# Optimization experiments

Measured on AMD Instinct MI355X. Metric: run time of the kernel, lower is better.

The kernel has to match this reference:

```python
import jax, jax.numpy as jnp
import numpy as np

# sigmas (defaults from the module)
VAR_0, VAR_A, VAR_B = 1.0, 1.0, 0.0

def V_phi(a, b, c):
    # default id_phi: (a, b, c) -> b, where Sigma = [[a, b], [b, c]]
    return b


def setup_inputs() -> dict:
    key = jax.random.key(0)
    kx, ky = jax.random.split(key)
    B, T, D = 128, 1024, 64
    dt = 1.0 / (T - 1)
    scale = np.sqrt(dt / D).astype(np.float32)
    # Brownian-like paths: increments ~ N(0, dt/D) so quadratic variation is O(1)
    # and the multiplicative kernel recurrence stays numerically bounded.
    X = jnp.cumsum(jax.random.normal(kx, (B, T, D), jnp.float32) * scale, axis=1)
    Y = jnp.cumsum(jax.random.normal(ky, (B, T, D), jnp.float32) * scale, axis=1)
    return {"X": X, "Y": Y}


def _kernel_same(dd):
    # dd: (b, T-1) = <dX_t, dX_t> / dt ; returns Kxx: (b, T)
    def step(k, d_t):
        k_new = k + (VAR_A * V_phi(k, k, k) + VAR_B) * d_t
        return k_new, k_new
    k0 = jnp.full((dd.shape[0],), VAR_0, dd.dtype)
    _, ks = jax.lax.scan(step, k0, dd.T)           # ks: (T-1, b)
    return jnp.concatenate([k0[None, :], ks], axis=0).T  # (b, T)


def reference(X, Y):
    bx, T, d = X.shape
    by = Y.shape[0]
    interval = jnp.linspace(0.0, 1.0, T).astype(X.dtype)
    dt = jnp.diff(interval)                         # (T-1,)
    dX = jnp.diff(X, axis=1)                        # (bx, T-1, d)
    dY = jnp.diff(Y, axis=1)                        # (by, T-1, d)

    dXdX = (dX * dX).sum(-1) / dt                   # (bx, T-1)
    dYdY = (dY * dY).sum(-1) / dt                   # (by, T-1)
    dXdY = jnp.einsum('itd,jtd->ijt', dX, dY) / dt  # (bx, by, T-1)

    Kxx = _kernel_same(dXdX)                        # (bx, T)
    Kyy = _kernel_same(dYdY)                        # (by, T)

    def step(k, inp):
        kxx_t, kyy_t, dxy_t = inp                   # (bx,), (by,), (bx, by)
        k_new = k + (VAR_A * V_phi(kxx_t[:, None], k, kyy_t[None, :]) + VAR_B) * dxy_t
        return k_new, k_new

    k0 = jnp.full((bx, by), VAR_0, X.dtype)
    xs = (Kxx[:, :-1].T, Kyy[:, :-1].T, jnp.moveaxis(dXdY, 2, 0))
    _, ks = jax.lax.scan(step, k0, xs)              # (T-1, bx, by)
    K = jnp.concatenate([k0[None], ks], axis=0)     # (T, bx, by)
    return jnp.moveaxis(K, 0, 2)                    # (bx, by, T)
```

## Files before the change

kernel.cpp:

```cpp
#include <hip/hip_runtime.h>

typedef __attribute__((ext_vector_type(8))) short short8;
typedef __attribute__((ext_vector_type(4))) float floatx4;

constexpr int BX    = 128;
constexpr int TT    = 1024;
constexpr int DDIM  = 64;
constexpr int NPAIR = BX * BX;
constexpr int LCH   = 16;
constexpr int NCH   = TT / LCH;
constexpr float DT_INV = 1023.0f;

__device__ __forceinline__ int sidxE(int row, int k) {
    return row * 64 + ((((k >> 3) ^ (row & 7)) << 3) | (k & 7));
}

__device__ __forceinline__ ushort f2bf(float f) {
    uint u = __builtin_bit_cast(uint, f);
    u += 0x7fffu + ((u >> 16) & 1u);
    return (ushort)(u >> 16);
}

__device__ __forceinline__ void cvt_store(ushort* hiP, ushort* loP, const float* v) {
    uint hw[4], lw[4];
#pragma unroll
    for (int p = 0; p < 4; ++p) {
        const ushort h0 = f2bf(v[2 * p]), h1 = f2bf(v[2 * p + 1]);
        const float r0 = v[2 * p]     - __builtin_bit_cast(float, (uint)h0 << 16);
        const float r1 = v[2 * p + 1] - __builtin_bit_cast(float, (uint)h1 << 16);
        const ushort l0 = f2bf(r0), l1 = f2bf(r1);
        hw[p] = (uint)h0 | ((uint)h1 << 16);
        lw[p] = (uint)l0 | ((uint)l1 << 16);
    }
    *(uint4*)hiP = make_uint4(hw[0], hw[1], hw[2], hw[3]);
    *(uint4*)loP = make_uint4(lw[0], lw[1], lw[2], lw[3]);
}

__device__ __forceinline__ void ld8(const float* p, float* dst) {
    const float4 a = *(const float4*)p;
    const float4 b = *(const float4*)(p + 4);
    dst[0] = a.x; dst[1] = a.y; dst[2] = a.z; dst[3] = a.w;
    dst[4] = b.x; dst[5] = b.y; dst[6] = b.z; dst[7] = b.w;
}

template<int WP>
__global__ __launch_bounds__(256, 2) void zchunk_kernel(const float* __restrict__ X,
                                                        const float* __restrict__ Y,
                                                        float* __restrict__ dst,
                                                        float* __restrict__ P)
{
    __shared__ __align__(16) ushort smXhi[2][64 * 64], smXlo[2][64 * 64];
    __shared__ __align__(16) ushort smYhi[2][32 * 64], smYlo[2][32 * 64];

    const int L    = (int)blockIdx.x;
    const int tile = (L >> 3) & 7;
    const int cz   = ((L >> 6) << 3) | (L & 7);
    const int i0 = (tile & 1) * 64;
    const int j0 = (tile >> 1) * 32;
    const int t0 = cz * LCH;
    const int tid  = (int)threadIdx.x;
    const int lane = tid & 63, w = tid >> 6, quad = lane >> 4, l15 = lane & 15;

    const int srow = tid >> 3;
    const int sseg = tid & 7;
    const float* xp0 = X + (size_t)(i0 + srow)      * TT * DDIM + sseg * 8;
    const float* xp1 = X + (size_t)(i0 + srow + 32) * TT * DDIM + sseg * 8;
    const float* yp  = Y + (size_t)(j0 + srow)      * TT * DDIM + sseg * 8;

    float cx0[8], cx1[8], cy[8];
    float rx0[2][8], rx1[2][8], ry[2][8];
    {
        const int sa = (t0 == 0) ? 0 : (t0 - 1);
        float pv0[8], pv1[8], pv2[8], d[8];
        ld8(xp0 + (size_t)t0 * DDIM, cx0);
        ld8(xp1 + (size_t)t0 * DDIM, cx1);
        ld8(yp  + (size_t)t0 * DDIM, cy);
        ld8(xp0 + (size_t)sa * DDIM, pv0);
        ld8(xp1 + (size_t)sa * DDIM, pv1);
        ld8(yp  + (size_t)sa * DDIM, pv2);
        ld8(xp0 + (size_t)(t0 + 1) * DDIM, rx0[1]);
        ld8(xp1 + (size_t)(t0 + 1) * DDIM, rx1[1]);
        ld8(yp  + (size_t)(t0 + 1) * DDIM, ry[1]);

#pragma unroll
        for (int k = 0; k < 8; ++k) d[k] = cx0[k] - pv0[k];
        cvt_store(&smXhi[0][sidxE(srow, sseg * 8)], &smXlo[0][sidxE(srow, sseg * 8)], d);
#pragma unroll
        for (int k = 0; k < 8; ++k) d[k] = cx1[k] - pv1[k];
        cvt_store(&smXhi[0][sidxE(srow + 32, sseg * 8)], &smXlo[0][sidxE(srow + 32, sseg * 8)], d);
#pragma unroll
        for (int k = 0; k < 8; ++k) d[k] = cy[k] - pv2[k];
        cvt_store(&smYhi[0][sidxE(srow, sseg * 8)], &smYlo[0][sidxE(srow, sseg * 8)], d);
    }

    float cum[2][4];
    uint  histP[2][4][8];
#pragma unroll
    for (int s = 0; s < 2; ++s)
#pragma unroll
        for (int r = 0; r < 4; ++r) cum[s][r] = 1.f;

    __syncthreads();

#pragma unroll
    for (int h = 0; h < LCH; ++h) {
        const int cur = h & 1;

        if (h + 2 < LCH) {
            const size_t u = (size_t)(t0 + h + 2) * DDIM;
            ld8(xp0 + u, rx0[h & 1]); ld8(xp1 + u, rx1[h & 1]); ld8(yp + u, ry[h & 1]);
        }

        short8 aHi[2], aLo[2];
#pragma unroll
        for (int kk = 0; kk < 2; ++kk) {
            const int e = sidxE(w * 16 + l15, kk * 32 + quad * 8);
            aHi[kk] = *(const short8*)&smXhi[cur][e];
            aLo[kk] = *(const short8*)&smXlo[cur][e];
        }

#pragma unroll
        for (int sub = 0; sub < 2; ++sub) {
            floatx4 acc = {0.f, 0.f, 0.f, 0.f};
#pragma unroll
            for (int kk = 0; kk < 2; ++kk) {
                const int e = sidxE(sub * 16 + l15, kk * 32 + quad * 8);
                const short8 bHi = *(const short8*)&smYhi[cur][e];
                const short8 bLo = *(const short8*)&smYlo[cur][e];
                acc = __builtin_amdgcn_mfma_f32_16x16x32_bf16(aLo[kk], bHi, acc, 0, 0, 0);
                acc = __builtin_amdgcn_mfma_f32_16x16x32_bf16(aHi[kk], bLo, acc, 0, 0, 0);
                acc = __builtin_amdgcn_mfma_f32_16x16x32_bf16(aHi[kk], bHi, acc, 0, 0, 0);
            }
#pragma unroll
            for (int r = 0; r < 4; ++r) {
                cum[sub][r] *= fmaf(acc[r], DT_INV, 1.f);
                const uint hb = (uint)f2bf(cum[sub][r]);
                if ((h & 1) == 0) histP[sub][r][h >> 1] = hb;
                else              histP[sub][r][h >> 1] |= (hb << 16);
            }
        }

        if (h + 1 < LCH) {
            const int nsel = (h + 1) & 1;
            float d[8];
#pragma unroll
            for (int k = 0; k < 8; ++k) d[k] = rx0[nsel][k] - cx0[k];
            cvt_store(&smXhi[cur ^ 1][sidxE(srow, sseg * 8)], &smXlo[cur ^ 1][sidxE(srow, sseg * 8)], d);
#pragma unroll
            for (int k = 0; k < 8; ++k) d[k] = rx1[nsel][k] - cx1[k];
            cvt_store(&smXhi[cur ^ 1][sidxE(srow + 32, sseg * 8)], &smXlo[cur ^ 1][sidxE(srow + 32, sseg * 8)], d);
#pragma unroll
            for (int k = 0; k < 8; ++k) d[k] = ry[nsel][k] - cy[k];
            cvt_store(&smYhi[cur ^ 1][sidxE(srow, sseg * 8)], &smYlo[cur ^ 1][sidxE(srow, sseg * 8)], d);
#pragma unroll
            for (int k = 0; k < 8; ++k) { cx0[k] = rx0[nsel][k]; cx1[k] = rx1[nsel][k]; cy[k] = ry[nsel][k]; }
            __syncthreads();
        }
    }

#pragma unroll
    for (int sub = 0; sub < 2; ++sub)
#pragma unroll
        for (int r = 0; r < 4; ++r) {
            const int pair = (i0 + w * 16 + quad * 4 + r) * BX + (j0 + sub * 16 + l15);
            P[(size_t)cz * NPAIR + pair] = cum[sub][r];
            float* o = WP ? (dst + ((size_t)cz * NPAIR + pair) * LCH)
                          : (dst + (size_t)pair * TT + t0);
#pragma unroll
            for (int q = 0; q < 4; ++q) {
                const uint u0 = histP[sub][r][2 * q];
                const uint u1 = histP[sub][r][2 * q + 1];
                *(float4*)(o + q * 4) = make_float4(
                    __builtin_bit_cast(float, u0 << 16),
                    __builtin_bit_cast(float, u0 & 0xffff0000u),
                    __builtin_bit_cast(float, u1 << 16),
                    __builtin_bit_cast(float, u1 & 0xffff0000u));
            }
        }
}

__global__ __launch_bounds__(256) void scanscale_w(float* __restrict__ out,
                                                   const float* __restrict__ W,
                                                   const float* __restrict__ P)
{
    __shared__ float pf[NCH][17];
    __shared__ float tot[16][17];

    const int p0  = (int)blockIdx.x * 16;
    const int tid = (int)threadIdx.x;
    const int p   = tid & 15;
    const int seg = tid >> 4;

    float v[4], e[4];
#pragma unroll
    for (int k = 0; k < 4; ++k)
        v[k] = P[(size_t)(seg * 4 + k) * NPAIR + p0 + p];
    e[0] = 1.f;
#pragma unroll
    for (int k = 1; k < 4; ++k) e[k] = e[k - 1] * v[k - 1];
    tot[seg][p] = e[3] * v[3];
    __syncthreads();

    float base = 1.f;
#pragma unroll
    for (int q = 0; q < 15; ++q)
        if (q < seg) base *= tot[q][p];
#pragma unroll
    for (int k = 0; k < 4; ++k)
        pf[seg * 4 + k][p] = base * e[k];
    __syncthreads();

    const int c  = tid >> 2;
    const int tq = tid & 3;
#pragma unroll
    for (int rb = 0; rb < 4; ++rb) {
        float4 w4[4];
        float  f[4];
#pragma unroll
        for (int u = 0; u < 4; ++u) {
            const int r = rb * 4 + u;
            f[u]  = pf[c][r];
            w4[u] = *(const float4*)(W + ((size_t)c * NPAIR + p0 + r) * LCH + tq * 4);
        }
#pragma unroll
        for (int u = 0; u < 4; ++u) {
            const int r = rb * 4 + u;
            *(float4*)(out + (size_t)(p0 + r) * TT + tid * 4) =
                make_float4(w4[u].x * f[u], w4[u].y * f[u],
                            w4[u].z * f[u], w4[u].w * f[u]);
        }
    }
}

__global__ __launch_bounds__(256) void scanscale_kernel(float* __restrict__ out,
                                                        const float* __restrict__ P)
{
    __shared__ float pf[16][NCH];
    const int p0  = (int)blockIdx.x * 16;
    const int tid = (int)threadIdx.x;

    if (tid < 16) {
        const int p = p0 + tid;
        float run = 1.f;
#pragma unroll 4
        for (int c = 0; c < NCH; ++c) {
            pf[tid][c] = run;
            run *= P[(size_t)c * NPAIR + p];
        }
    }
    __syncthreads();

    const int pp  = tid >> 4;
    const int col = tid & 15;
    float* row = out + (size_t)(p0 + pp) * TT;
#pragma unroll
    for (int seg = 0; seg < 16; ++seg) {
        const int t = seg * 64 + col * 4;
        const float f = pf[pp][t >> 4];
        float4 v = *(float4*)(row + t);
        v.x *= f; v.y *= f; v.z *= f; v.w *= f;
        *(float4*)(row + t) = v;
    }
}

extern "C" void kernel_launch(void* const* d_in, const int* in_sizes, int n_in,
                              void* d_out, int out_size, void* d_ws, size_t ws_size,
                              hipStream_t stream)
{
    const float* X = (const float*)d_in[0];
    const float* Y = (const float*)d_in[1];
    float* out = (float*)d_out;
    float* P   = (float*)d_ws;
    float* W   = (float*)d_ws + (size_t)NCH * NPAIR;

    const size_t need = ((size_t)NCH * NPAIR + (size_t)NPAIR * TT) * sizeof(float);
    if (ws_size >= need) {
        zchunk_kernel<1><<<dim3(512), 256, 0, stream>>>(X, Y, W, P);
        scanscale_w<<<dim3(NPAIR / 16), 256, 0, stream>>>(out, W, P);
    } else {
        zchunk_kernel<0><<<dim3(512), 256, 0, stream>>>(X, Y, out, P);
        scanscale_kernel<<<dim3(NPAIR / 16), 256, 0, stream>>>(out, P);
    }
}
```

Before: 156.9 us.

## Shrink zchunk tiles to 32x32, double block count, rework scanscale store loop

The chunk kernel now uses 32x32 pair tiles instead of 64x32, with one 16x16 MFMA output per wave, and launches 1024 blocks with a higher occupancy bound. This raises parallelism and cuts register and LDS use per block, at the cost of loading each X/Y increment twice as often. The scanscale_w store loop is restructured so each wave handles 16 chunks with one float4 per lane. The bf16 hi/lo split now uses the HIP packed conversion intrinsics.

```diff
diff --git a/kernel.cpp b/kernel.cpp
--- a/kernel.cpp
+++ b/kernel.cpp
@@ -1,4 +1,5 @@
 #include <hip/hip_runtime.h>
+#include <hip/hip_bf16.h>
 
 typedef __attribute__((ext_vector_type(8))) short short8;
 typedef __attribute__((ext_vector_type(4))) float floatx4;
@@ -25,12 +26,12 @@
     uint hw[4], lw[4];
 #pragma unroll
     for (int p = 0; p < 4; ++p) {
-        const ushort h0 = f2bf(v[2 * p]), h1 = f2bf(v[2 * p + 1]);
-        const float r0 = v[2 * p]     - __builtin_bit_cast(float, (uint)h0 << 16);
-        const float r1 = v[2 * p + 1] - __builtin_bit_cast(float, (uint)h1 << 16);
-        const ushort l0 = f2bf(r0), l1 = f2bf(r1);
-        hw[p] = (uint)h0 | ((uint)h1 << 16);
-        lw[p] = (uint)l0 | ((uint)l1 << 16);
+        const __hip_bfloat162 h = __float22bfloat162_rn(make_float2(v[2 * p], v[2 * p + 1]));
+        const float r0 = v[2 * p]     - __bfloat162float(h.x);
+        const float r1 = v[2 * p + 1] - __bfloat162float(h.y);
+        const __hip_bfloat162 l = __float22bfloat162_rn(make_float2(r0, r1));
+        hw[p] = (uint)__bfloat16_as_ushort(h.x) | ((uint)__bfloat16_as_ushort(h.y) << 16);
+        lw[p] = (uint)__bfloat16_as_ushort(l.x) | ((uint)__bfloat16_as_ushort(l.y) << 16);
     }
     *(uint4*)hiP = make_uint4(hw[0], hw[1], hw[2], hw[3]);
     *(uint4*)loP = make_uint4(lw[0], lw[1], lw[2], lw[3]);
@@ -44,61 +45,53 @@
 }
 
 template<int WP>
-__global__ __launch_bounds__(256, 2) void zchunk_kernel(const float* __restrict__ X,
+__global__ __launch_bounds__(256, 4) void zchunk_kernel(const float* __restrict__ X,
                                                         const float* __restrict__ Y,
                                                         float* __restrict__ dst,
                                                         float* __restrict__ P)
 {
-    __shared__ __align__(16) ushort smXhi[2][64 * 64], smXlo[2][64 * 64];
+    __shared__ __align__(16) ushort smXhi[2][32 * 64], smXlo[2][32 * 64];
     __shared__ __align__(16) ushort smYhi[2][32 * 64], smYlo[2][32 * 64];
 
     const int L    = (int)blockIdx.x;
-    const int tile = (L >> 3) & 7;
-    const int cz   = ((L >> 6) << 3) | (L & 7);
-    const int i0 = (tile & 1) * 64;
-    const int j0 = (tile >> 1) * 32;
+    const int tile = (L >> 3) & 15;
+    const int cz   = ((L >> 7) << 3) | (L & 7);
+    const int i0 = (tile & 3) * 32;
+    const int j0 = (tile >> 2) * 32;
     const int t0 = cz * LCH;
     const int tid  = (int)threadIdx.x;
     const int lane = tid & 63, w = tid >> 6, quad = lane >> 4, l15 = lane & 15;
+    const int wr = w >> 1, wc = w & 1;
 
     const int srow = tid >> 3;
     const int sseg = tid & 7;
-    const float* xp0 = X + (size_t)(i0 + srow)      * TT * DDIM + sseg * 8;
-    const float* xp1 = X + (size_t)(i0 + srow + 32) * TT * DDIM + sseg * 8;
-    const float* yp  = Y + (size_t)(j0 + srow)      * TT * DDIM + sseg * 8;
-
-    float cx0[8], cx1[8], cy[8];
-    float rx0[2][8], rx1[2][8], ry[2][8];
+    const float* xp = X + (size_t)(i0 + srow) * TT * DDIM + sseg * 8;
+    const float* yp = Y + (size_t)(j0 + srow) * TT * DDIM + sseg * 8;
+
+    float cx[8], cy[8];
+    float rx[2][8], ry[2][8];
     {
         const int sa = (t0 == 0) ? 0 : (t0 - 1);
-        float pv0[8], pv1[8], pv2[8], d[8];
-        ld8(xp0 + (size_t)t0 * DDIM, cx0);
-        ld8(xp1 + (size_t)t0 * DDIM, cx1);
-        ld8(yp  + (size_t)t0 * DDIM, cy);
-        ld8(xp0 + (size_t)sa * DDIM, pv0);
-        ld8(xp1 + (size_t)sa * DDIM, pv1);
-        ld8(yp  + (size_t)sa * DDIM, pv2);
-        ld8(xp0 + (size_t)(t0 + 1) * DDIM, rx0[1]);
-        ld8(xp1 + (size_t)(t0 + 1) * DDIM, rx1[1]);
-        ld8(yp  + (size_t)(t0 + 1) * DDIM, ry[1]);
-
-#pragma unroll
-        for (int k = 0; k < 8; ++k) d[k] = cx0[k] - pv0[k];
+        float pvx[8], pvy[8], d[8];
+        ld8(xp + (size_t)t0 * DDIM, cx);
+        ld8(yp + (size_t)t0 * DDIM, cy);
+        ld8(xp + (size_t)sa * DDIM, pvx);
+        ld8(yp + (size_t)sa * DDIM, pvy);
+        ld8(xp + (size_t)(t0 + 1) * DDIM, rx[1]);
+        ld8(yp + (size_t)(t0 + 1) * DDIM, ry[1]);
+
+#pragma unroll
+        for (int k = 0; k < 8; ++k) d[k] = cx[k] - pvx[k];
         cvt_store(&smXhi[0][sidxE(srow, sseg * 8)], &smXlo[0][sidxE(srow, sseg * 8)], d);
 #pragma unroll
-        for (int k = 0; k < 8; ++k) d[k] = cx1[k] - pv1[k];
-        cvt_store(&smXhi[0][sidxE(srow + 32, sseg * 8)], &smXlo[0][sidxE(srow + 32, sseg * 8)], d);
-#pragma unroll
-        for (int k = 0; k < 8; ++k) d[k] = cy[k] - pv2[k];
+        for (int k = 0; k < 8; ++k) d[k] = cy[k] - pvy[k];
         cvt_store(&smYhi[0][sidxE(srow, sseg * 8)], &smYlo[0][sidxE(srow, sseg * 8)], d);
     }
 
-    float cum[2][4];
-    uint  histP[2][4][8];
-#pragma unroll
-    for (int s = 0; s < 2; ++s)
-#pragma unroll
-        for (int r = 0; r < 4; ++r) cum[s][r] = 1.f;
+    float cum[4];
+    uint  histP[4][8];
+#pragma unroll
+    for (int r = 0; r < 4; ++r) cum[r] = 1.f;
 
     __syncthreads();
 
@@ -108,75 +101,67 @@
 
         if (h + 2 < LCH) {
             const size_t u = (size_t)(t0 + h + 2) * DDIM;
-            ld8(xp0 + u, rx0[h & 1]); ld8(xp1 + u, rx1[h & 1]); ld8(yp + u, ry[h & 1]);
+            ld8(xp + u, rx[h & 1]); ld8(yp + u, ry[h & 1]);
         }
 
         short8 aHi[2], aLo[2];
 #pragma unroll
         for (int kk = 0; kk < 2; ++kk) {
-            const int e = sidxE(w * 16 + l15, kk * 32 + quad * 8);
+            const int e = sidxE(wr * 16 + l15, kk * 32 + quad * 8);
             aHi[kk] = *(const short8*)&smXhi[cur][e];
             aLo[kk] = *(const short8*)&smXlo[cur][e];
         }
 
-#pragma unroll
-        for (int sub = 0; sub < 2; ++sub) {
-            floatx4 acc = {0.f, 0.f, 0.f, 0.f};
-#pragma unroll
-            for (int kk = 0; kk < 2; ++kk) {
-                const int e = sidxE(sub * 16 + l15, kk * 32 + quad * 8);
-                const short8 bHi = *(const short8*)&smYhi[cur][e];
-                const short8 bLo = *(const short8*)&smYlo[cur][e];
-                acc = __builtin_amdgcn_mfma_f32_16x16x32_bf16(aLo[kk], bHi, acc, 0, 0, 0);
-                acc = __builtin_amdgcn_mfma_f32_16x16x32_bf16(aHi[kk], bLo, acc, 0, 0, 0);
-                acc = __builtin_amdgcn_mfma_f32_16x16x32_bf16(aHi[kk], bHi, acc, 0, 0, 0);
-            }
-#pragma unroll
-            for (int r = 0; r < 4; ++r) {
-                cum[sub][r] *= fmaf(acc[r], DT_INV, 1.f);
-                const uint hb = (uint)f2bf(cum[sub][r]);
-                if ((h & 1) == 0) histP[sub][r][h >> 1] = hb;
-                else              histP[sub][r][h >> 1] |= (hb << 16);
-            }
+        floatx4 acc = {0.f, 0.f, 0.f, 0.f};
+#pragma unroll
+        for (int kk = 0; kk < 2; ++kk) {
+            const int e = sidxE(wc * 16 + l15, kk * 32 + quad * 8);
+            const short8 bHi = *(const short8*)&smYhi[cur][e];
+            const short8 bLo = *(const short8*)&smYlo[cur][e];
+            acc = __builtin_amdgcn_mfma_f32_16x16x32_bf16(aLo[kk], bHi, acc, 0, 0, 0);
+            acc = __builtin_amdgcn_mfma_f32_16x16x32_bf16(aHi[kk], bLo, acc, 0, 0, 0);
+            acc = __builtin_amdgcn_mfma_f32_16x16x32_bf16(aHi[kk], bHi, acc, 0, 0, 0);
+        }
+#pragma unroll
+        for (int r = 0; r < 4; ++r) {
+            cum[r] *= fmaf(acc[r], DT_INV, 1.f);
+            const uint hb = (uint)f2bf(cum[r]);
+            if ((h & 1) == 0) histP[r][h >> 1] = hb;
+            else              histP[r][h >> 1] |= (hb << 16);
         }
 
         if (h + 1 < LCH) {
             const int nsel = (h + 1) & 1;
             float d[8];
 #pragma unroll
-            for (int k = 0; k < 8; ++k) d[k] = rx0[nsel][k] - cx0[k];
+            for (int k = 0; k < 8; ++k) d[k] = rx[nsel][k] - cx[k];
             cvt_store(&smXhi[cur ^ 1][sidxE(srow, sseg * 8)], &smXlo[cur ^ 1][sidxE(srow, sseg * 8)], d);
-#pragma unroll
-            for (int k = 0; k < 8; ++k) d[k] = rx1[nsel][k] - cx1[k];
-            cvt_store(&smXhi[cur ^ 1][sidxE(srow + 32, sseg * 8)], &smXlo[cur ^ 1][sidxE(srow + 32, sseg * 8)], d);
 #pragma unroll
             for (int k = 0; k < 8; ++k) d[k] = ry[nsel][k] - cy[k];
             cvt_store(&smYhi[cur ^ 1][sidxE(srow, sseg * 8)], &smYlo[cur ^ 1][sidxE(srow, sseg * 8)], d);
 #pragma unroll
-            for (int k = 0; k < 8; ++k) { cx0[k] = rx0[nsel][k]; cx1[k] = rx1[nsel][k]; cy[k] = ry[nsel][k]; }
+            for (int k = 0; k < 8; ++k) { cx[k] = rx[nsel][k]; cy[k] = ry[nsel][k]; }
             __syncthreads();
         }
     }
 
 #pragma unroll
-    for (int sub = 0; sub < 2; ++sub)
-#pragma unroll
-        for (int r = 0; r < 4; ++r) {
-            const int pair = (i0 + w * 16 + quad * 4 + r) * BX + (j0 + sub * 16 + l15);
-            P[(size_t)cz * NPAIR + pair] = cum[sub][r];
-            float* o = WP ? (dst + ((size_t)cz * NPAIR + pair) * LCH)
-                          : (dst + (size_t)pair * TT + t0);
-#pragma unroll
-            for (int q = 0; q < 4; ++q) {
-                const uint u0 = histP[sub][r][2 * q];
-                const uint u1 = histP[sub][r][2 * q + 1];
-                *(float4*)(o + q * 4) = make_float4(
-                    __builtin_bit_cast(float, u0 << 16),
-                    __builtin_bit_cast(float, u0 & 0xffff0000u),
-                    __builtin_bit_cast(float, u1 << 16),
-                    __builtin_bit_cast(float, u1 & 0xffff0000u));
-            }
-        }
+    for (int r = 0; r < 4; ++r) {
+        const int pair = (i0 + wr * 16 + quad * 4 + r) * BX + (j0 + wc * 16 + l15);
+        P[(size_t)cz * NPAIR + pair] = cum[r];
+        float* o = WP ? (dst + ((size_t)cz * NPAIR + pair) * LCH)
+                      : (dst + (size_t)pair * TT + t0);
+#pragma unroll
+        for (int q = 0; q < 4; ++q) {
+            const uint u0 = histP[r][2 * q];
+            const uint u1 = histP[r][2 * q + 1];
+            *(float4*)(o + q * 4) = make_float4(
+                __builtin_bit_cast(float, u0 << 16),
+                __builtin_bit_cast(float, u0 & 0xffff0000u),
+                __builtin_bit_cast(float, u1 << 16),
+                __builtin_bit_cast(float, u1 & 0xffff0000u));
+        }
+    }
 }
 
 __global__ __launch_bounds__(256) void scanscale_w(float* __restrict__ out,
@@ -210,25 +195,18 @@
         pf[seg * 4 + k][p] = base * e[k];
     __syncthreads();
 
-    const int c  = tid >> 2;
-    const int tq = tid & 3;
-#pragma unroll
-    for (int rb = 0; rb < 4; ++rb) {
-        float4 w4[4];
-        float  f[4];
-#pragma unroll
-        for (int u = 0; u < 4; ++u) {
-            const int r = rb * 4 + u;
-            f[u]  = pf[c][r];
-            w4[u] = *(const float4*)(W + ((size_t)c * NPAIR + p0 + r) * LCH + tq * 4);
-        }
-#pragma unroll
-        for (int u = 0; u < 4; ++u) {
-            const int r = rb * 4 + u;
-            *(float4*)(out + (size_t)(p0 + r) * TT + tid * 4) =
-                make_float4(w4[u].x * f[u], w4[u].y * f[u],
-                            w4[u].z * f[u], w4[u].w * f[u]);
-        }
+    const int wv = tid >> 6;
+    const int l  = tid & 63;
+    const int pr = l >> 2;
+    const int tq = l & 3;
+    float* orow = out + (size_t)(p0 + pr) * TT + tq * 4;
+#pragma unroll 2
+    for (int k = 0; k < 16; ++k) {
+        const int c = wv * 16 + k;
+        const float4 w4 = *(const float4*)(W + ((size_t)c * NPAIR + p0 + pr) * LCH + tq * 4);
+        const float f = pf[c][pr];
+        *(float4*)(orow + (size_t)c * LCH) =
+            make_float4(w4.x * f, w4.y * f, w4.z * f, w4.w * f);
     }
 }
 
@@ -275,10 +253,10 @@
 
     const size_t need = ((size_t)NCH * NPAIR + (size_t)NPAIR * TT) * sizeof(float);
     if (ws_size >= need) {
-        zchunk_kernel<1><<<dim3(512), 256, 0, stream>>>(X, Y, W, P);
+        zchunk_kernel<1><<<dim3(1024), 256, 0, stream>>>(X, Y, W, P);
         scanscale_w<<<dim3(NPAIR / 16), 256, 0, stream>>>(out, W, P);
     } else {
-        zchunk_kernel<0><<<dim3(512), 256, 0, stream>>>(X, Y, out, P);
+        zchunk_kernel<0><<<dim3(1024), 256, 0, stream>>>(X, Y, out, P);
         scanscale_kernel<<<dim3(NPAIR / 16), 256, 0, stream>>>(out, P);
     }
 }
```

Measured after the change: 176.3 us. 1.12x slower.

## Store chunk history as packed bf16, deepen prefetch, stage via LDS in scan

Applied to the files above, without the earlier changes.

The intermediate per-chunk history buffer W is now written as packed bf16 pairs rather than expanded fp32. This halves the bytes written by the chunk kernel and read back by the scan-scale kernel. The scan kernel stages W through a padded shared-memory tile so global reads are coalesced before writing scaled fp32 output. The global prefetch depth in the chunk kernel goes from 2 to 4 timesteps, which costs more registers. The split-bf16 conversion also switches to the HIP bf16 intrinsics.

```diff
diff --git a/kernel.cpp b/kernel.cpp
--- a/kernel.cpp
+++ b/kernel.cpp
@@ -1,4 +1,5 @@
 #include <hip/hip_runtime.h>
+#include <hip/hip_bf16.h>
 
 typedef __attribute__((ext_vector_type(8))) short short8;
 typedef __attribute__((ext_vector_type(4))) float floatx4;
@@ -25,12 +26,12 @@
     uint hw[4], lw[4];
 #pragma unroll
     for (int p = 0; p < 4; ++p) {
-        const ushort h0 = f2bf(v[2 * p]), h1 = f2bf(v[2 * p + 1]);
-        const float r0 = v[2 * p]     - __builtin_bit_cast(float, (uint)h0 << 16);
-        const float r1 = v[2 * p + 1] - __builtin_bit_cast(float, (uint)h1 << 16);
-        const ushort l0 = f2bf(r0), l1 = f2bf(r1);
-        hw[p] = (uint)h0 | ((uint)h1 << 16);
-        lw[p] = (uint)l0 | ((uint)l1 << 16);
+        const __hip_bfloat162 h = __float22bfloat162_rn(make_float2(v[2 * p], v[2 * p + 1]));
+        const float r0 = v[2 * p]     - __bfloat162float(h.x);
+        const float r1 = v[2 * p + 1] - __bfloat162float(h.y);
+        const __hip_bfloat162 l = __float22bfloat162_rn(make_float2(r0, r1));
+        hw[p] = (uint)__bfloat16_as_ushort(h.x) | ((uint)__bfloat16_as_ushort(h.y) << 16);
+        lw[p] = (uint)__bfloat16_as_ushort(l.x) | ((uint)__bfloat16_as_ushort(l.y) << 16);
     }
     *(uint4*)hiP = make_uint4(hw[0], hw[1], hw[2], hw[3]);
     *(uint4*)loP = make_uint4(lw[0], lw[1], lw[2], lw[3]);
@@ -46,7 +47,8 @@
 template<int WP>
 __global__ __launch_bounds__(256, 2) void zchunk_kernel(const float* __restrict__ X,
                                                         const float* __restrict__ Y,
-                                                        float* __restrict__ dst,
+                                                        float* __restrict__ dstF,
+                                                        uint*  __restrict__ Wp,
                                                         float* __restrict__ P)
 {
     __shared__ __align__(16) ushort smXhi[2][64 * 64], smXlo[2][64 * 64];
@@ -68,7 +70,7 @@
     const float* yp  = Y + (size_t)(j0 + srow)      * TT * DDIM + sseg * 8;
 
     float cx0[8], cx1[8], cy[8];
-    float rx0[2][8], rx1[2][8], ry[2][8];
+    float rx0[4][8], rx1[4][8], ry[4][8];
     {
         const int sa = (t0 == 0) ? 0 : (t0 - 1);
         float pv0[8], pv1[8], pv2[8], d[8];
@@ -78,9 +80,12 @@
         ld8(xp0 + (size_t)sa * DDIM, pv0);
         ld8(xp1 + (size_t)sa * DDIM, pv1);
         ld8(yp  + (size_t)sa * DDIM, pv2);
-        ld8(xp0 + (size_t)(t0 + 1) * DDIM, rx0[1]);
-        ld8(xp1 + (size_t)(t0 + 1) * DDIM, rx1[1]);
-        ld8(yp  + (size_t)(t0 + 1) * DDIM, ry[1]);
+#pragma unroll
+        for (int s = 1; s <= 3; ++s) {
+            ld8(xp0 + (size_t)(t0 + s) * DDIM, rx0[s]);
+            ld8(xp1 + (size_t)(t0 + s) * DDIM, rx1[s]);
+            ld8(yp  + (size_t)(t0 + s) * DDIM, ry[s]);
+        }
 
 #pragma unroll
         for (int k = 0; k < 8; ++k) d[k] = cx0[k] - pv0[k];
@@ -106,9 +111,9 @@
     for (int h = 0; h < LCH; ++h) {
         const int cur = h & 1;
 
-        if (h + 2 < LCH) {
-            const size_t u = (size_t)(t0 + h + 2) * DDIM;
-            ld8(xp0 + u, rx0[h & 1]); ld8(xp1 + u, rx1[h & 1]); ld8(yp + u, ry[h & 1]);
+        if (h + 4 < LCH) {
+            const size_t u = (size_t)(t0 + h + 4) * DDIM;
+            ld8(xp0 + u, rx0[h & 3]); ld8(xp1 + u, rx1[h & 3]); ld8(yp + u, ry[h & 3]);
         }
 
         short8 aHi[2], aLo[2];
@@ -141,7 +146,7 @@
         }
 
         if (h + 1 < LCH) {
-            const int nsel = (h + 1) & 1;
+            const int nsel = (h + 1) & 3;
             float d[8];
 #pragma unroll
             for (int k = 0; k < 8; ++k) d[k] = rx0[nsel][k] - cx0[k];
@@ -164,25 +169,33 @@
         for (int r = 0; r < 4; ++r) {
             const int pair = (i0 + w * 16 + quad * 4 + r) * BX + (j0 + sub * 16 + l15);
             P[(size_t)cz * NPAIR + pair] = cum[sub][r];
-            float* o = WP ? (dst + ((size_t)cz * NPAIR + pair) * LCH)
-                          : (dst + (size_t)pair * TT + t0);
-#pragma unroll
-            for (int q = 0; q < 4; ++q) {
-                const uint u0 = histP[sub][r][2 * q];
-                const uint u1 = histP[sub][r][2 * q + 1];
-                *(float4*)(o + q * 4) = make_float4(
-                    __builtin_bit_cast(float, u0 << 16),
-                    __builtin_bit_cast(float, u0 & 0xffff0000u),
-                    __builtin_bit_cast(float, u1 << 16),
-                    __builtin_bit_cast(float, u1 & 0xffff0000u));
+            if (WP) {
+                uint* o = Wp + ((size_t)cz * NPAIR + pair) * 8;
+                *(uint4*)o       = make_uint4(histP[sub][r][0], histP[sub][r][1],
+                                              histP[sub][r][2], histP[sub][r][3]);
+                *(uint4*)(o + 4) = make_uint4(histP[sub][r][4], histP[sub][r][5],
+                                              histP[sub][r][6], histP[sub][r][7]);
+            } else {
+                float* o = dstF + (size_t)pair * TT + t0;
+#pragma unroll
+                for (int q = 0; q < 4; ++q) {
+                    const uint u0 = histP[sub][r][2 * q];
+                    const uint u1 = histP[sub][r][2 * q + 1];
+                    *(float4*)(o + q * 4) = make_float4(
+                        __builtin_bit_cast(float, u0 << 16),
+                        __builtin_bit_cast(float, u0 & 0xffff0000u),
+                        __builtin_bit_cast(float, u1 << 16),
+                        __builtin_bit_cast(float, u1 & 0xffff0000u));
+                }
             }
         }
 }
 
 __global__ __launch_bounds__(256) void scanscale_w(float* __restrict__ out,
-                                                   const float* __restrict__ W,
+                                                   const uint* __restrict__ W,
                                                    const float* __restrict__ P)
 {
+    __shared__ uint2 tileW[NCH * 65];
     __shared__ float pf[NCH][17];
     __shared__ float tot[16][17];
 
@@ -208,27 +221,27 @@
 #pragma unroll
     for (int k = 0; k < 4; ++k)
         pf[seg * 4 + k][p] = base * e[k];
-    __syncthreads();
-
-    const int c  = tid >> 2;
-    const int tq = tid & 3;
-#pragma unroll
-    for (int rb = 0; rb < 4; ++rb) {
-        float4 w4[4];
-        float  f[4];
-#pragma unroll
-        for (int u = 0; u < 4; ++u) {
-            const int r = rb * 4 + u;
-            f[u]  = pf[c][r];
-            w4[u] = *(const float4*)(W + ((size_t)c * NPAIR + p0 + r) * LCH + tq * 4);
-        }
-#pragma unroll
-        for (int u = 0; u < 4; ++u) {
-            const int r = rb * 4 + u;
-            *(float4*)(out + (size_t)(p0 + r) * TT + tid * 4) =
-                make_float4(w4[u].x * f[u], w4[u].y * f[u],
-                            w4[u].z * f[u], w4[u].w * f[u]);
-        }
+
+    const int wv = tid >> 6, l = tid & 63;
+    const int pr = l >> 2, tb = l & 3;
+#pragma unroll
+    for (int k = 0; k < 16; ++k) {
+        const int c = wv * 16 + k;
+        tileW[c * 65 + pr * 4 + tb] =
+            *(const uint2*)(W + ((size_t)c * NPAIR + p0 + pr) * 8 + tb * 2);
+    }
+    __syncthreads();
+
+    const int c2 = tid >> 2, q2 = tid & 3;
+#pragma unroll 2
+    for (int r = 0; r < 16; ++r) {
+        const uint2 u = tileW[c2 * 65 + r * 4 + q2];
+        const float f = pf[c2][r];
+        *(float4*)(out + (size_t)(p0 + r) * TT + tid * 4) = make_float4(
+            __builtin_bit_cast(float, u.x << 16) * f,
+            __builtin_bit_cast(float, u.x & 0xffff0000u) * f,
+            __builtin_bit_cast(float, u.y << 16) * f,
+            __builtin_bit_cast(float, u.y & 0xffff0000u) * f);
     }
 }
 
@@ -271,14 +284,14 @@
     const float* Y = (const float*)d_in[1];
     float* out = (float*)d_out;
     float* P   = (float*)d_ws;
-    float* W   = (float*)d_ws + (size_t)NCH * NPAIR;
-
-    const size_t need = ((size_t)NCH * NPAIR + (size_t)NPAIR * TT) * sizeof(float);
+    uint*  W   = (uint*)((float*)d_ws + (size_t)NCH * NPAIR);
+
+    const size_t need = (size_t)NCH * NPAIR * (4 + 32);
     if (ws_size >= need) {
-        zchunk_kernel<1><<<dim3(512), 256, 0, stream>>>(X, Y, W, P);
+        zchunk_kernel<1><<<dim3(512), 256, 0, stream>>>(X, Y, out, W, P);
         scanscale_w<<<dim3(NPAIR / 16), 256, 0, stream>>>(out, W, P);
     } else {
-        zchunk_kernel<0><<<dim3(512), 256, 0, stream>>>(X, Y, out, P);
+        zchunk_kernel<0><<<dim3(512), 256, 0, stream>>>(X, Y, out, W, P);
         scanscale_kernel<<<dim3(NPAIR / 16), 256, 0, stream>>>(out, P);
     }
 }
```

New measurement: 149.0 us. 1.05x faster.
